# Optimization experiments

Measured on AMD Instinct MI355X. Metric: run time of the kernel, lower is better.

## Reference

```python
import jax, jax.numpy as jnp
import numpy as np

WS = 7    # window size
SS = 3    # shift size
NH = 6    # num heads
C = 192   # dim
HID = 768 # mlp hidden = 4*dim


def _rel_index():
    c = np.stack(np.meshgrid(np.arange(WS), np.arange(WS), indexing='ij')).reshape(2, -1)
    r = (c[:, :, None] - c[:, None, :]).transpose(1, 2, 0)
    r[..., 0] += WS - 1
    r[..., 1] += WS - 1
    r[..., 0] *= 2 * WS - 1
    return r.sum(-1)  # (49, 49) int


def _ln(x, g, b):
    m = jnp.mean(x, -1, keepdims=True)
    v = jnp.var(x, -1, keepdims=True)
    return (x - m) / jnp.sqrt(v + 1e-5) * g + b


def _wpart(x):
    B, H, W, c = x.shape
    return x.reshape(B, H // WS, WS, W // WS, WS, c).transpose(0, 1, 3, 2, 4, 5).reshape(-1, WS * WS, c)


def _wrev(w, H, W):
    B = w.shape[0] // ((H // WS) * (W // WS))
    return w.reshape(B, H // WS, W // WS, WS, WS, -1).transpose(0, 1, 3, 2, 4, 5).reshape(B, H, W, -1)


def setup_inputs() -> dict:
    key = jax.random.key(0)
    ks = jax.random.split(key, 40)
    it = iter(range(40))
    def nrm(shape, s=0.02):
        return jax.random.normal(ks[next(it)], shape, jnp.float32) * s
    B, H, W = 16, 56, 56
    L = H * W
    d = dict(se=nrm((B, L, C), 1.0), de=nrm((B, L, C), 1.0), co=nrm((B, L, C), 1.0))
    # shifted-window attention mask, exactly as Swin builds it
    img = np.zeros((1, H, W, 1), np.float32)
    cnt = 0
    for hs in (slice(0, -WS), slice(-WS, -SS), slice(-SS, None)):
        for cs in (slice(0, -WS), slice(-WS, -SS), slice(-SS, None)):
            img[:, hs, cs, :] = cnt
            cnt += 1
    mw = np.asarray(_wpart(jnp.asarray(img))).reshape(-1, WS * WS)  # (nW, 49)
    am = mw[:, None, :] - mw[:, :, None]
    d['mask_matrix'] = jnp.asarray(np.where(am != 0, -100.0, 0.0).astype(np.float32))
    d.update(
        n1se_g=jnp.ones(C), n1se_b=jnp.zeros(C), n1de_g=jnp.ones(C), n1de_b=jnp.zeros(C),
        rpb_table=nrm(((2 * WS - 1) ** 2, NH)),
        vse_w=nrm((2 * C, C)), vse_b=jnp.zeros(C), vde_w=nrm((2 * C, C)), vde_b=jnp.zeros(C),
        qk_w=nrm((C, 2 * C)), qk_b=jnp.zeros(2 * C),
        pse_w=nrm((C, C)), pse_b=jnp.zeros(C), pde_w=nrm((C, C)), pde_b=jnp.zeros(C),
        n2se_g=jnp.ones(C), n2se_b=jnp.zeros(C), n2de_g=jnp.ones(C), n2de_b=jnp.zeros(C),
        mse_w1=nrm((C, HID)), mse_b1=jnp.zeros(HID), mse_w2=nrm((HID, C)), mse_b2=jnp.zeros(C),
        mde_w1=nrm((C, HID)), mde_b1=jnp.zeros(HID), mde_w2=nrm((HID, C)), mde_b2=jnp.zeros(C),
        H=H, W=W)
    return d


def reference(se, de, co, mask_matrix,
              n1se_g, n1se_b, n1de_g, n1de_b, rpb_table,
              vse_w, vse_b, vde_w, vde_b, qk_w, qk_b,
              pse_w, pse_b, pde_w, pde_b,
              n2se_g, n2se_b, n2de_g, n2de_b,
              mse_w1, mse_b1, mse_w2, mse_b2,
              mde_w1, mde_b1, mde_w2, mde_b2,
              H, W):
    B, L, Cd = se.shape
    dh = Cd // NH
    scale = dh ** -0.5
    sc_se, sc_de = se, de
    se_n = _ln(se, n1se_g, n1se_b).reshape(B, H, W, Cd)
    de_n = _ln(de, n1de_g, n1de_b).reshape(B, H, W, Cd)
    co_n = co.reshape(B, H, W, Cd)  # co is not normed in the torch block
    # cyclic shift (H, W divisible by WS -> zero padding)
    se_s = jnp.roll(se_n, (-SS, -SS), (1, 2))
    de_s = jnp.roll(de_n, (-SS, -SS), (1, 2))
    co_s = jnp.roll(co_n, (-SS, -SS), (1, 2))
    sw, dw, cw = _wpart(se_s), _wpart(de_s), _wpart(co_s)  # (B_, N, C)
    B_, N, _ = sw.shape
    v_se = (jnp.concatenate([sw, cw], -1) @ vse_w + vse_b).reshape(B_, N, NH, dh).transpose(0, 2, 1, 3)
    v_de = (jnp.concatenate([dw, cw], -1) @ vde_w + vde_b).reshape(B_, N, NH, dh).transpose(0, 2, 1, 3)
    qk = (cw @ qk_w + qk_b).reshape(B_, N, 2, NH, dh).transpose(2, 0, 3, 1, 4)
    q, k = qk[0] * scale, qk[1]
    attn = jnp.einsum('bhnd,bhmd->bhnm', q, k)  # (B_, NH, N, N)
    bias = rpb_table[_rel_index().reshape(-1)].reshape(N, N, NH).transpose(2, 0, 1)
    attn = attn + bias[None]
    nW = mask_matrix.shape[0]
    attn = (attn.reshape(B_ // nW, nW, NH, N, N) + mask_matrix[None, :, None]).reshape(B_, NH, N, N)
    attn = jax.nn.softmax(attn, -1)
    se_o = jnp.einsum('bhnm,bhmd->bhnd', attn, v_se).transpose(0, 2, 1, 3).reshape(B_, N, Cd) @ pse_w + pse_b
    de_o = jnp.einsum('bhnm,bhmd->bhnd', attn, v_de).transpose(0, 2, 1, 3).reshape(B_, N, Cd) @ pde_w + pde_b
    se_r = jnp.roll(_wrev(se_o, H, W), (SS, SS), (1, 2)).reshape(B, L, Cd)
    de_r = jnp.roll(_wrev(de_o, H, W), (SS, SS), (1, 2)).reshape(B, L, Cd)
    se_out = sc_se + se_r
    de_out = sc_de + de_r
    se_out = se_out + (jax.nn.gelu(_ln(se_out, n2se_g, n2se_b) @ mse_w1 + mse_b1, approximate=False) @ mse_w2 + mse_b2)
    de_out = de_out + (jax.nn.gelu(_ln(de_out, n2de_g, n2de_b) @ mde_w1 + mde_b1, approximate=False) @ mde_w2 + mde_b2)
    return (se_out, de_out)
```

## Files before the change

kernel.cpp:

```cpp
#include <hip/hip_runtime.h>
#include <hip/hip_bf16.h>
#include <math.h>
#include <stdint.h>

typedef __hip_bfloat16 bf16;
typedef __attribute__((ext_vector_type(8))) short short8;
typedef __attribute__((ext_vector_type(4))) float f32x4;

#define B_SZ   16
#define HH     56
#define WW2    56
#define L_TOK  3136
#define C_DIM  192
#define NH_    6
#define DH     32
#define WS_    7
#define SS_    3
#define NW     49
#define NWIN   64
#define BWIN   (B_SZ*NWIN)
#define TOK    (BWIN*NW)
#define HID_   768

__device__ __forceinline__ float b2f(bf16 x){ return __bfloat162float(x); }
__device__ __forceinline__ bf16  f2b(float x){ return __float2bfloat16(x); }
__device__ __forceinline__ short f2bs(float x){ bf16 h = __float2bfloat16(x); return *reinterpret_cast<short*>(&h); }

__device__ __forceinline__ void gload16(const void* g, void* l) {
    __builtin_amdgcn_global_load_lds(
        (const __attribute__((address_space(1))) void*)(uintptr_t)g,
        (__attribute__((address_space(3))) void*)(uintptr_t)l, 16, 0, 0);
}

__device__ __forceinline__ float wave_sum64(float v){
    #pragma unroll
    for (int off = 32; off > 0; off >>= 1) v += __shfl_xor(v, off, 64);
    return v;
}

__global__ void prep_kernel(const float* __restrict__ se, const float* __restrict__ de,
                            const float* __restrict__ co,
                            const float* __restrict__ g1s, const float* __restrict__ b1s,
                            const float* __restrict__ g1d, const float* __restrict__ b1d,
                            bf16* __restrict__ sw, bf16* __restrict__ dw, bf16* __restrict__ cw)
{
    int t   = blockIdx.x;
    int tid = threadIdx.x;
    int b_  = t / NW, n = t % NW;
    int b   = b_ / NWIN, w = b_ % NWIN;
    int wh  = w >> 3, wwi = w & 7;
    int i   = n / WS_, j = n % WS_;
    int hs  = wh*WS_ + i, ws = wwi*WS_ + j;
    int hsrc = hs + SS_; if (hsrc >= HH)  hsrc -= HH;
    int wsrc = ws + SS_; if (wsrc >= WW2) wsrc -= WW2;
    long src = ((long)(b*L_TOK + hsrc*WW2 + wsrc)) * C_DIM;
    long dst = (long)t * C_DIM;

    {
        float x0 = se[src+tid], x1 = se[src+tid+64], x2 = se[src+tid+128];
        float s  = wave_sum64(x0+x1+x2);
        float ss = wave_sum64(x0*x0 + x1*x1 + x2*x2);
        float mean = s * (1.0f/192.0f);
        float var  = ss * (1.0f/192.0f) - mean*mean;
        float rstd = rsqrtf(var + 1e-5f);
        sw[dst+tid]     = f2b((x0-mean)*rstd*g1s[tid]     + b1s[tid]);
        sw[dst+tid+64]  = f2b((x1-mean)*rstd*g1s[tid+64]  + b1s[tid+64]);
        sw[dst+tid+128] = f2b((x2-mean)*rstd*g1s[tid+128] + b1s[tid+128]);
    }
    {
        float x0 = de[src+tid], x1 = de[src+tid+64], x2 = de[src+tid+128];
        float s  = wave_sum64(x0+x1+x2);
        float ss = wave_sum64(x0*x0 + x1*x1 + x2*x2);
        float mean = s * (1.0f/192.0f);
        float var  = ss * (1.0f/192.0f) - mean*mean;
        float rstd = rsqrtf(var + 1e-5f);
        dw[dst+tid]     = f2b((x0-mean)*rstd*g1d[tid]     + b1d[tid]);
        dw[dst+tid+64]  = f2b((x1-mean)*rstd*g1d[tid+64]  + b1d[tid+64]);
        dw[dst+tid+128] = f2b((x2-mean)*rstd*g1d[tid+128] + b1d[tid+128]);
    }
    cw[dst+tid]     = f2b(co[src+tid]);
    cw[dst+tid+64]  = f2b(co[src+tid+64]);
    cw[dst+tid+128] = f2b(co[src+tid+128]);
}

__global__ __launch_bounds__(256)
void wconv(const float* w0,const float* w1,const float* w2,const float* w3,const float* w4,
           const float* w5,const float* w6,const float* w7,const float* w8, short* dst)
{
    const float* src; int K, N; long doff;
    switch (blockIdx.y) {
      case 0: src=w0; K=384; N=192; doff=0;      break;
      case 1: src=w1; K=384; N=192; doff=73728;  break;
      case 2: src=w2; K=192; N=384; doff=147456; break;
      case 3: src=w3; K=192; N=192; doff=221184; break;
      case 4: src=w4; K=192; N=192; doff=258048; break;
      case 5: src=w5; K=192; N=768; doff=294912; break;
      case 6: src=w6; K=768; N=192; doff=442368; break;
      case 7: src=w7; K=192; N=768; doff=589824; break;
      default:src=w8; K=768; N=192; doff=737280; break;
    }
    int nblk = (K>>5)*(N>>6);
    int bid = blockIdx.x;
    if (bid >= nblk) return;
    int kb = bid / (N>>6), nb = bid % (N>>6);
    __shared__ float tile[32][65];
    int tid = threadIdx.x;
    #pragma unroll
    for (int it = 0; it < 8; ++it) {
        int idx = tid + it*256;
        int r = idx >> 6, c = idx & 63;
        tile[r][c] = src[(long)(kb*32 + r)*N + nb*64 + c];
    }
    __syncthreads();
    int lane = tid & 63, nl = tid >> 6;
    short8 v;
    #pragma unroll
    for (int j = 0; j < 8; ++j)
        v[j] = f2bs(tile[(lane>>4)*8 + j][nl*16 + (lane&15)]);
    long nig = (long)nb*4 + nl;
    *(short8*)(dst + doff + (((long)kb*(N>>4) + nig)*64 + lane)*8) = v;
}

template<int MODE, bool DUAL, int MR16>
__global__ __launch_bounds__(384)
void fgemm2(const bf16* __restrict__ A1, const bf16* __restrict__ A2, int K1, int K,
            const short* __restrict__ wf, const float* __restrict__ bias, int Nn,
            bf16* __restrict__ out, bf16* __restrict__ out2,
            const bf16* __restrict__ A1b, const bf16* __restrict__ A2b,
            const short* __restrict__ wfB, const float* __restrict__ biasB,
            bf16* __restrict__ outB, int nxblk)
{
    __shared__ short AsF[2][MR16][64][8];
    const int MROWS = MR16 * 16;
    const int MPW   = MR16 / 2;
    int tid = threadIdx.x;
    int wid = tid >> 6, lane = tid & 63;
    int wr = (wid >= 3) ? 1 : 0, wc = wid - wr*3;
    int l15 = lane & 15, g = lane >> 4;

    int bx = blockIdx.x;
    const bf16 *A1p = A1, *A2p = A2; const short* wfp = wf;
    const float* biasp = bias; bf16* outp = out;
    if (DUAL && bx >= nxblk) {
        bx -= nxblk; A1p = A1b; A2p = A2b; wfp = wfB; biasp = biasB; outp = outB;
    }
    int row0 = bx * MROWS, col0 = blockIdx.y * 192;
    const int ntiles = Nn >> 4;

    f32x4 acc[MPW][4];
    #pragma unroll
    for (int m = 0; m < MPW; m++)
        #pragma unroll
        for (int n = 0; n < 4; n++)
            acc[m][n] = (f32x4){0.f,0.f,0.f,0.f};

    int nk = K >> 5;
    #define STAGE(buf_, k0_) {                                                   \
        int colk = (k0_) + (g << 3);                                             \
        const bf16* asrc = (colk < K1) ? A1p : A2p;                              \
        int kc = (colk < K1) ? colk : colk - K1;                                 \
        if (wid < MR16)                                                          \
            gload16(asrc + (long)(row0 + wid*16 + l15)*K1 + kc,                  \
                    &AsF[buf_][wid][0][0]);                                      \
        if (MR16 == 8 && wid < 2)                                                \
            gload16(asrc + (long)(row0 + (6+wid)*16 + l15)*K1 + kc,              \
                    &AsF[buf_][(MR16==8 ? 6+wid : 0)][0][0]);                    \
    }

    STAGE(0, 0);
    __syncthreads();
    for (int t = 0; t < nk; ++t) {
        int buf = t & 1;
        if (t + 1 < nk) STAGE(buf ^ 1, (t+1) << 5);
        short8 af[MPW], bf4[4];
        #pragma unroll
        for (int m = 0; m < MPW; m++) af[m] = *((short8*)&AsF[buf][wr*MPW + m][lane][0]);
        const short* wbase = wfp + (((long)t*ntiles + (col0>>4) + wc*4)*64 + lane)*8;
        #pragma unroll
        for (int n = 0; n < 4; n++) bf4[n] = *(const short8*)(wbase + n*512);
        #pragma unroll
        for (int m = 0; m < MPW; m++)
            #pragma unroll
            for (int n = 0; n < 4; n++)
                acc[m][n] = __builtin_amdgcn_mfma_f32_16x16x32_bf16(af[m], bf4[n], acc[m][n], 0, 0, 0);
        __syncthreads();
    }
    #undef STAGE

    #pragma unroll
    for (int m = 0; m < MPW; m++) {
        #pragma unroll
        for (int rr = 0; rr < 4; rr++) {
            int t = row0 + wr*(MROWS/2) + m*16 + g*4 + rr;
            #pragma unroll
            for (int n2 = 0; n2 < 4; n2++) {
                int oc = col0 + wc*64 + n2*16 + l15;
                float v = acc[m][n2][rr] + biasp[oc];
                if (MODE == 0) {
                    outp[(long)t*Nn + oc] = f2b(v);
                } else if (MODE == 1) {
                    int b_ = t / NW, n = t % NW;
                    if (oc < C_DIM) {
                        int head = oc >> 5, d = oc & 31;
                        outp[(((long)b_*NH_ + head)*NW + n)*DH + d] = f2b(v * 0.17677669529663687f);
                    } else {
                        int och = oc - C_DIM;
                        int head = och >> 5, d = och & 31;
                        out2[(((long)b_*NH_ + head)*NW + n)*DH + d] = f2b(v);
                    }
                } else {
                    int b_ = t / NW, n = t % NW;
                    int head = oc >> 5, d = oc & 31;
                    outp[(((long)b_*NH_ + head)*NW + n)*DH + d] = f2b(v);
                }
            }
        }
    }
}

__global__ __launch_bounds__(384)
void pproj_ln2(const bf16* __restrict__ A, const short* __restrict__ wf,
               const float* __restrict__ bias, const float* __restrict__ res,
               const float* __restrict__ g2, const float* __restrict__ b2,
               bf16* __restrict__ x1o, bf16* __restrict__ xno,
               const bf16* __restrict__ Ab, const short* __restrict__ wfB,
               const float* __restrict__ biasB, const float* __restrict__ resB,
               const float* __restrict__ g2B, const float* __restrict__ b2B,
               bf16* __restrict__ x1oB, bf16* __restrict__ xnoB,
               int nxblk)
{
    __shared__ short AsFp[2][8][64][8];
    __shared__ float part[128][3][2];

    int tid = threadIdx.x;
    int wid = tid >> 6, lane = tid & 63;
    int wr = (wid >= 3) ? 1 : 0, wc = wid - wr*3;
    int l15 = lane & 15, g = lane >> 4;

    int bx = blockIdx.x;
    const bf16* Ap = A; const short* wfp = wf; const float* biasp = bias;
    const float* resp = res; const float* g2p = g2; const float* b2p = b2;
    bf16* x1p = x1o; bf16* xnp = xno;
    if (bx >= nxblk) {
        bx -= nxblk; Ap = Ab; wfp = wfB; biasp = biasB; resp = resB;
        g2p = g2B; b2p = b2B; x1p = x1oB; xnp = xnoB;
    }
    int row0 = bx * 128;

    f32x4 acc[4][4];
    #pragma unroll
    for (int m = 0; m < 4; m++)
        #pragma unroll
        for (int n = 0; n < 4; n++)
            acc[m][n] = (f32x4){0.f,0.f,0.f,0.f};

    #define PSTAGE(buf_, k0_) {                                                  \
        int colk = (k0_) + (g << 3);                                             \
        if (wid < 6)                                                             \
            gload16(Ap + (long)(row0 + wid*16 + l15)*C_DIM + colk,               \
                    &AsFp[buf_][wid][0][0]);                                     \
        if (wid < 2)                                                             \
            gload16(Ap + (long)(row0 + (6+wid)*16 + l15)*C_DIM + colk,           \
                    &AsFp[buf_][6+wid][0][0]);                                   \
    }

    PSTAGE(0, 0);
    __syncthreads();
    for (int t = 0; t < 6; ++t) {
        int buf = t & 1;
        if (t + 1 < 6) PSTAGE(buf ^ 1, (t+1) << 5);
        short8 af[4], bf4[4];
        #pragma unroll
        for (int m = 0; m < 4; m++)
            af[m] = *((short8*)&AsFp[buf][wr*4 + m][lane][0]);
        const short* wbase = wfp + (((long)t*12 + wc*4)*64 + lane)*8;
        #pragma unroll
        for (int n = 0; n < 4; n++) bf4[n] = *(const short8*)(wbase + n*512);
        #pragma unroll
        for (int m = 0; m < 4; m++)
            #pragma unroll
            for (int n = 0; n < 4; n++)
                acc[m][n] = __builtin_amdgcn_mfma_f32_16x16x32_bf16(af[m], bf4[n], acc[m][n], 0, 0, 0);
        __syncthreads();
    }
    #undef PSTAGE

    float bias4[4], g24[4], b24[4];
    #pragma unroll
    for (int n2 = 0; n2 < 4; n2++) {
        int oc = wc*64 + n2*16 + l15;
        bias4[n2] = biasp[oc]; g24[n2] = g2p[oc]; b24[n2] = b2p[oc];
    }

    int gtv[4][4];
    #pragma unroll
    for (int m = 0; m < 4; m++) {
        #pragma unroll
        for (int rr = 0; rr < 4; rr++) {
            int t = row0 + wr*64 + m*16 + g*4 + rr;
            int b_ = t / NW, n = t - b_*NW;
            int w = b_ & (NWIN-1), b = b_ >> 6;
            int hs = (w >> 3)*WS_ + n/WS_;
            int wsf = (w & 7)*WS_ + n % WS_;
            int h = hs + SS_;  if (h >= HH)  h -= HH;
            int wc2 = wsf + SS_; if (wc2 >= WW2) wc2 -= WW2;
            int gt = b*L_TOK + h*WW2 + wc2;
            gtv[m][rr] = gt;
            int lrow = wr*64 + m*16 + g*4 + rr;
            float ps = 0.f, pss = 0.f;
            #pragma unroll
            for (int n2 = 0; n2 < 4; n2++) {
                int oc = wc*64 + n2*16 + l15;
                float x1 = resp[(long)gt*C_DIM + oc] + acc[m][n2][rr] + bias4[n2];
                acc[m][n2][rr] = x1;
                x1p[(long)gt*C_DIM + oc] = f2b(x1);
                ps += x1; pss += x1*x1;
            }
            ps  += __shfl_xor(ps, 1);  pss += __shfl_xor(pss, 1);
            ps  += __shfl_xor(ps, 2);  pss += __shfl_xor(pss, 2);
            ps  += __shfl_xor(ps, 4);  pss += __shfl_xor(pss, 4);
            ps  += __shfl_xor(ps, 8);  pss += __shfl_xor(pss, 8);
            if (l15 == 0) {
                part[lrow][wc][0] = ps;
                part[lrow][wc][1] = pss;
            }
        }
    }
    __syncthreads();

    #pragma unroll
    for (int m = 0; m < 4; m++) {
        #pragma unroll
        for (int rr = 0; rr < 4; rr++) {
            int lrow = wr*64 + m*16 + g*4 + rr;
            int gt = gtv[m][rr];
            float s  = part[lrow][0][0] + part[lrow][1][0] + part[lrow][2][0];
            float ss = part[lrow][0][1] + part[lrow][1][1] + part[lrow][2][1];
            float mean = s * (1.0f/192.0f);
            float var  = ss * (1.0f/192.0f) - mean*mean;
            float rstd = rsqrtf(var + 1e-5f);
            #pragma unroll
            for (int n2 = 0; n2 < 4; n2++) {
                int oc = wc*64 + n2*16 + l15;
                xnp[(long)gt*C_DIM + oc] = f2b((acc[m][n2][rr] - mean)*rstd*g24[n2] + b24[n2]);
            }
        }
    }
}

__global__ __launch_bounds__(384)
void mlp_fused3(const bf16* __restrict__ xn, const short* __restrict__ w1f,
                const short* __restrict__ w2f,
                const float* __restrict__ b1, const float* __restrict__ b2,
                const bf16* __restrict__ x1, float* __restrict__ dout,
                const bf16* __restrict__ xnB, const short* __restrict__ w1B,
                const short* __restrict__ w2B,
                const float* __restrict__ b1B, const float* __restrict__ b2B,
                const bf16* __restrict__ x1B, float* __restrict__ doutB,
                int nxblk)
{
    __shared__ short xnF[24*512];
    __shared__ short hidS[2][24*512];

    int tid = threadIdx.x;
    int wv = tid >> 6, lane = tid & 63;
    int l15 = lane & 15, g = lane >> 4;

    int bx = blockIdx.x;
    const bf16* xnp = xn; const short* w1p = w1f; const short* w2p = w2f;
    const float* b1p = b1; const float* b2p = b2;
    const bf16* x1p = x1; float* doutp = dout;
    if (bx >= nxblk) {
        bx -= nxblk; xnp = xnB; w1p = w1B; w2p = w2B; b1p = b1B; b2p = b2B;
        x1p = x1B; doutp = doutB;
    }
    int row0 = bx * 64;

    #pragma unroll
    for (int p = 0; p < 4; ++p) {
        int pp = wv*4 + p;
        int a = pp / 6, kb = pp % 6;
        gload16(xnp + (long)(row0 + 16*a + l15)*C_DIM + 32*kb + 8*g,
                xnF + (a*6 + kb)*512);
    }
    __syncthreads();

    f32x4 ad[4][2], au[4][2];
    #pragma unroll
    for (int m = 0; m < 4; m++)
        #pragma unroll
        for (int n = 0; n < 2; n++)
            ad[m][n] = (f32x4){0.f,0.f,0.f,0.f};

    #define UP_SLICE(s_) {                                                       \
        _Pragma("unroll")                                                        \
        for (int m = 0; m < 4; m++)                                              \
            _Pragma("unroll")                                                    \
            for (int n = 0; n < 2; n++)                                          \
                au[m][n] = (f32x4){0.f,0.f,0.f,0.f};                             \
        _Pragma("unroll")                                                        \
        for (int kb = 0; kb < 6; ++kb) {                                         \
            short8 af[4];                                                        \
            _Pragma("unroll")                                                    \
            for (int m = 0; m < 4; m++)                                          \
                af[m] = *(short8*)(xnF + (m*6 + kb)*512 + lane*8);               \
            _Pragma("unroll")                                                    \
            for (int n = 0; n < 2; n++) {                                        \
                short8 bfv = *(const short8*)(w1p + (((long)kb*48 + 12*(s_) + 2*wv + n)*64 + lane)*8); \
                _Pragma("unroll")                                                \
                for (int m = 0; m < 4; m++)                                      \
                    au[m][n] = __builtin_amdgcn_mfma_f32_16x16x32_bf16(af[m], bfv, au[m][n], 0, 0, 0); \
            }                                                                    \
        }                                                                        \
    }

    #define SCATTER(s_, buf_) {                                                  \
        _Pragma("unroll")                                                        \
        for (int n = 0; n < 2; n++) {                                            \
            int hc = 32*wv + 16*n + l15;                                         \
            float bb = b1p[192*(s_) + hc];                                       \
            int kb2 = hc >> 5;                                                   \
            int Lhi = 16 * ((hc >> 3) & 3);                                      \
            int j = hc & 7;                                                      \
            _Pragma("unroll")                                                    \
            for (int m = 0; m < 4; m++) {                                        \
                _Pragma("unroll")                                                \
                for (int rr = 0; rr < 4; rr++) {                                 \
                    float v = au[m][n][rr] + bb;                                 \
                    float gl = 0.5f * v * (1.0f + erff(v * 0.70710678118654752f)); \
                    int L = (4*g + rr) + Lhi;                                    \
                    hidS[buf_][(m*6 + kb2)*512 + L*8 + j] = f2bs(gl);            \
                }                                                                \
            }                                                                    \
        }                                                                        \
    }

    #define DOWN_SLICE(s_, buf_) {                                               \
        _Pragma("unroll")                                                        \
        for (int kb = 0; kb < 6; ++kb) {                                         \
            short8 hf[4];                                                        \
            _Pragma("unroll")                                                    \
            for (int m = 0; m < 4; m++)                                          \
                hf[m] = *(short8*)(&hidS[buf_][(m*6 + kb)*512] + lane*8);        \
            _Pragma("unroll")                                                    \
            for (int n = 0; n < 2; n++) {                                        \
                short8 bfv = *(const short8*)(w2p + ((((long)(6*(s_) + kb))*12 + 2*wv + n)*64 + lane)*8); \
                _Pragma("unroll")                                                \
                for (int m = 0; m < 4; m++)                                      \
                    ad[m][n] = __builtin_amdgcn_mfma_f32_16x16x32_bf16(hf[m], bfv, ad[m][n], 0, 0, 0); \
            }                                                                    \
        }                                                                        \
    }

    UP_SLICE(0);
    SCATTER(0, 0);
    __syncthreads();
    UP_SLICE(1);
    DOWN_SLICE(0, 0);
    SCATTER(1, 1);
    __syncthreads();
    UP_SLICE(2);
    DOWN_SLICE(1, 1);
    SCATTER(2, 0);
    __syncthreads();
    UP_SLICE(3);
    DOWN_SLICE(2, 0);
    SCATTER(3, 1);
    __syncthreads();
    DOWN_SLICE(3, 1);

    #undef UP_SLICE
    #undef SCATTER
    #undef DOWN_SLICE

    #pragma unroll
    for (int m = 0; m < 4; m++) {
        #pragma unroll
        for (int rr = 0; rr < 4; rr++) {
            int t = row0 + 16*m + 4*g + rr;
            long goff = (long)t*C_DIM;
            #pragma unroll
            for (int n = 0; n < 2; n++) {
                int oc = 32*wv + 16*n + l15;
                float v = ad[m][n][rr] + b2p[oc];
                doutp[goff + oc] = b2f(x1p[goff + oc]) + v;
            }
        }
    }
}

#define BM 128
#define BN 64

template<int MODE>
__global__ __launch_bounds__(256)
void mgemm(const bf16* __restrict__ A1, const bf16* __restrict__ A2, int K1, int K,
           const float* __restrict__ W, const float* __restrict__ bias, int Nn,
           bf16* __restrict__ out, bf16* __restrict__ out2,
           const float* __restrict__ res_src, const bf16* __restrict__ prj,
           int t0, float* __restrict__ dout)
{
    __shared__ short AsF[8][64][8];
    __shared__ short BsF[4][64][8];
    int tid  = threadIdx.x;
    int wid  = tid >> 6, lane = tid & 63;
    int wr   = wid >> 1, wc = wid & 1;
    int row0 = blockIdx.x * BM, col0 = blockIdx.y * BN;

    f32x4 acc[4][2];
    #pragma unroll
    for (int m = 0; m < 4; m++)
        #pragma unroll
        for (int n = 0; n < 2; n++)
            acc[m][n] = (f32x4){0.f, 0.f, 0.f, 0.f};

    int ar = tid >> 2, akseg = tid & 3;
    int bc = tid & 63, bk8 = tid >> 6;

    for (int k0 = 0; k0 < K; k0 += 32) {
        {
            int col = k0 + akseg*8;
            const bf16* asrc = (col < K1) ? A1 : A2;
            int akc = (col < K1) ? col : col - K1;
            #pragma unroll
            for (int rr = 0; rr < 2; rr++) {
                int r = ar + rr*64;
                short8 av = *(const short8*)(asrc + (long)(row0 + r)*K1 + akc);
                *((short8*)&AsF[r >> 4][(r & 15) + (akseg << 4)][0]) = av;
            }
        }
        {
            short8 bv;
            #pragma unroll
            for (int j = 0; j < 8; j++)
                bv[j] = f2bs(W[(long)(k0 + bk8*8 + j)*Nn + col0 + bc]);
            *((short8*)&BsF[bc >> 4][(bc & 15) + (bk8 << 4)][0]) = bv;
        }
        __syncthreads();
        short8 af[4], bfr[2];
        #pragma unroll
        for (int m = 0; m < 4; m++) af[m]  = *((short8*)&AsF[wr*4 + m][lane][0]);
        #pragma unroll
        for (int n = 0; n < 2; n++) bfr[n] = *((short8*)&BsF[wc*2 + n][lane][0]);
        #pragma unroll
        for (int m = 0; m < 4; m++)
            #pragma unroll
            for (int n = 0; n < 2; n++)
                acc[m][n] = __builtin_amdgcn_mfma_f32_16x16x32_bf16(af[m], bfr[n], acc[m][n], 0, 0, 0);
        __syncthreads();
    }

    #pragma unroll
    for (int m = 0; m < 4; m++) {
        #pragma unroll
        for (int rr = 0; rr < 4; rr++) {
            int t = row0 + wr*64 + m*16 + (lane >> 4)*4 + rr;
            if (MODE == 4) {
                int tg = t0 + t;
                int b = tg / L_TOK, l = tg % L_TOK;
                int h = l / WW2, wcol = l % WW2;
                int hp = h - SS_;    if (hp < 0) hp += HH;
                int wp = wcol - SS_; if (wp < 0) wp += WW2;
                int b_ = b*NWIN + (hp/WS_)*8 + (wp/WS_);
                int n  = (hp%WS_)*WS_ + (wp%WS_);
                long wsoff = ((long)b_*NW + n)*C_DIM;
                long goff  = (long)tg*C_DIM;
                #pragma unroll
                for (int n2 = 0; n2 < 2; n2++) {
                    int oc = col0 + wc*32 + n2*16 + (lane & 15);
                    float v = acc[m][n2][rr] + bias[oc];
                    dout[goff + oc] = res_src[goff + oc] + b2f(prj[wsoff + oc]) + v;
                }
            } else {
                #pragma unroll
                for (int n2 = 0; n2 < 2; n2++) {
                    int oc = col0 + wc*32 + n2*16 + (lane & 15);
                    float v = acc[m][n2][rr] + bias[oc];
                    if (MODE == 0) {
                        out[(long)t*Nn + oc] = f2b(v);
                    } else if (MODE == 1) {
                        int b_ = t / NW, n = t % NW;
                        if (oc < C_DIM) {
                            int head = oc >> 5, d = oc & 31;
                            out[(((long)b_*NH_ + head)*NW + n)*DH + d] = f2b(v * 0.17677669529663687f);
                        } else {
                            int och = oc - C_DIM;
                            int head = och >> 5, d = och & 31;
                            out2[(((long)b_*NH_ + head)*NW + n)*DH + d] = f2b(v);
                        }
                    } else if (MODE == 2) {
                        int b_ = t / NW, n = t % NW;
                        int head = oc >> 5, d = oc & 31;
                        out[(((long)b_*NH_ + head)*NW + n)*DH + d] = f2b(v);
                    } else {
                        float g2 = 0.5f * v * (1.0f + erff(v * 0.70710678118654752f));
                        out[(long)t*Nn + oc] = f2b(g2);
                    }
                }
            }
        }
    }
}

#define PSTR 72
#define VSTR 72

__global__ __launch_bounds__(128)
void attn_mfma(const bf16* __restrict__ qb, const bf16* __restrict__ kb,
               const bf16* __restrict__ vse, const bf16* __restrict__ vde,
               const float* __restrict__ rpb,
               bf16* __restrict__ ose, bf16* __restrict__ ode)
{
    __shared__ float rpbs[169*NH_];
    __shared__ short P[2][64][PSTR];
    __shared__ short VTs[2][32][VSTR];
    __shared__ short VTd[2][32][VSTR];
    int tid = threadIdx.x, wid = tid >> 6, lane = tid & 63;
    for (int i = tid; i < 169*NH_; i += 128) rpbs[i] = rpb[i];
    __syncthreads();

    int bh = blockIdx.x*2 + wid;
    int b_ = bh / NH_, head = bh % NH_;
    int w = b_ & (NWIN-1);
    int wh = w >> 3, ww = w & 7;
    long base = (long)bh * (NW*DH);
    int l15 = lane & 15, g = lane >> 4;
    int j0 = lane >> 2, seg = lane & 3;

    short8 qf[4], kf[4], va_[4], vb_[4];
    #pragma unroll
    for (int mi = 0; mi < 4; mi++) {
        int r = l15 + 16*mi; if (r > 48) r = 48;
        qf[mi] = *(const short8*)(qb + base + r*DH + 8*g);
    }
    #pragma unroll
    for (int ni = 0; ni < 4; ni++) {
        int r = l15 + 16*ni; if (r > 48) r = 48;
        kf[ni] = *(const short8*)(kb + base + r*DH + 8*g);
    }
    #pragma unroll
    for (int it = 0; it < 4; ++it) {
        int j = j0 + 16*it;
        va_[it] = (short8){0,0,0,0,0,0,0,0};
        vb_[it] = (short8){0,0,0,0,0,0,0,0};
        if (j < NW) {
            va_[it] = *(const short8*)(vse + base + j*DH + seg*8);
            vb_[it] = *(const short8*)(vde + base + j*DH + seg*8);
        }
    }

    f32x4 sA[4][4];
    #pragma unroll
    for (int mi = 0; mi < 4; mi++)
        #pragma unroll
        for (int ni = 0; ni < 4; ni++)
            sA[mi][ni] = (f32x4){0.f,0.f,0.f,0.f};
    #pragma unroll
    for (int mi = 0; mi < 4; mi++)
        #pragma unroll
        for (int ni = 0; ni < 4; ni++)
            sA[mi][ni] = __builtin_amdgcn_mfma_f32_16x16x32_bf16(qf[mi], kf[ni], sA[mi][ni], 0, 0, 0);

    #pragma unroll
    for (int it = 0; it < 4; ++it) {
        int j = j0 + 16*it;
        #pragma unroll
        for (int s2 = 0; s2 < 8; ++s2) {
            VTs[wid][seg*8 + s2][j] = va_[it][s2];
            VTd[wid][seg*8 + s2][j] = vb_[it][s2];
        }
    }

    int jv[4], j7r_[4], j7c_[4], jrh_[4], jrc_[4];
    #pragma unroll
    for (int ni = 0; ni < 4; ++ni) {
        int j = 16*ni + l15;
        jv[ni] = (j < NW);
        int a = (j*37) >> 8; int c = j - 7*a;
        j7r_[ni] = a; j7c_[ni] = c;
        int jh = wh*7 + a, jw = ww*7 + c;
        jrh_[ni] = (jh >= 49) + (jh >= 53);
        jrc_[ni] = (jw >= 49) + (jw >= 53);
    }

    #pragma unroll
    for (int mi = 0; mi < 4; mi++) {
        #pragma unroll
        for (int rr = 0; rr < 4; rr++) {
            int i = 16*mi + 4*g + rr;
            int iv = (i < NW);
            int i7r = (i*37) >> 8; int i7c = i - 7*i7r;
            int ih = wh*7 + i7r, iw = ww*7 + i7c;
            int irh = (ih >= 49) + (ih >= 53), irc = (iw >= 49) + (iw >= 53);
            float e[4], sum = 0.f;
            #pragma unroll
            for (int ni = 0; ni < 4; ni++) {
                float sv;
                if (iv && jv[ni]) {
                    int ri = (i7r - j7r_[ni] + 6)*13 + (i7c - j7c_[ni] + 6);
                    float msk = (irh == jrh_[ni] && irc == jrc_[ni]) ? 0.f : -100.f;
                    sv = sA[mi][ni][rr] + rpbs[ri*NH_ + head] + msk;
                } else {
                    sv = -1e30f;
                }
                e[ni] = __expf(sv); sum += e[ni];
            }
            sum += __shfl_xor(sum, 1);
            sum += __shfl_xor(sum, 2);
            sum += __shfl_xor(sum, 4);
            sum += __shfl_xor(sum, 8);
            float inv = 1.0f / sum;
            #pragma unroll
            for (int ni = 0; ni < 4; ni++)
                P[wid][i][16*ni + l15] = f2bs(e[ni] * inv);
        }
    }
    __syncthreads();

    f32x4 o1[4][2], o2[4][2];
    #pragma unroll
    for (int mi = 0; mi < 4; mi++)
        #pragma unroll
        for (int di = 0; di < 2; di++) {
            o1[mi][di] = (f32x4){0.f,0.f,0.f,0.f};
            o2[mi][di] = (f32x4){0.f,0.f,0.f,0.f};
        }
    #pragma unroll
    for (int mi = 0; mi < 4; mi++) {
        #pragma unroll
        for (int kk = 0; kk < 2; kk++) {
            short8 ap = *((short8*)&P[wid][16*mi + l15][kk*32 + 8*g]);
            #pragma unroll
            for (int di = 0; di < 2; di++) {
                short8 bv1 = *((short8*)&VTs[wid][16*di + l15][kk*32 + 8*g]);
                o1[mi][di] = __builtin_amdgcn_mfma_f32_16x16x32_bf16(ap, bv1, o1[mi][di], 0, 0, 0);
                short8 bv2 = *((short8*)&VTd[wid][16*di + l15][kk*32 + 8*g]);
                o2[mi][di] = __builtin_amdgcn_mfma_f32_16x16x32_bf16(ap, bv2, o2[mi][di], 0, 0, 0);
            }
        }
    }

    #pragma unroll
    for (int mi = 0; mi < 4; mi++) {
        #pragma unroll
        for (int rr = 0; rr < 4; rr++) {
            int i = 16*mi + 4*g + rr;
            if (i < NW) {
                long ob = ((long)b_*NW + i)*C_DIM + head*DH;
                #pragma unroll
                for (int di = 0; di < 2; di++) {
                    ose[ob + 16*di + l15] = f2b(o1[mi][di][rr]);
                    ode[ob + 16*di + l15] = f2b(o2[mi][di][rr]);
                }
            }
        }
    }
}

__global__ void resid_ln2_kernel(const float* __restrict__ se, const float* __restrict__ de,
                                 const bf16* __restrict__ pse, const bf16* __restrict__ pde,
                                 const float* __restrict__ g2s, const float* __restrict__ bb2s,
                                 const float* __restrict__ g2d, const float* __restrict__ bb2d,
                                 bf16* __restrict__ xns, bf16* __restrict__ xnd)
{
    int t = blockIdx.x, tid = threadIdx.x;
    int b = t / L_TOK, l = t % L_TOK;
    int h = l / WW2, wc = l % WW2;
    int hp = h - SS_;  if (hp < 0) hp += HH;
    int wp = wc - SS_; if (wp < 0) wp += WW2;
    int b_ = b*NWIN + (hp/WS_)*8 + (wp/WS_);
    int n  = (hp%WS_)*WS_ + (wp%WS_);
    long wsoff = ((long)b_*NW + n)*C_DIM;
    long off   = (long)t*C_DIM;
    {
        float x0 = se[off+tid]     + b2f(pse[wsoff+tid]);
        float x1 = se[off+tid+64]  + b2f(pse[wsoff+tid+64]);
        float x2 = se[off+tid+128] + b2f(pse[wsoff+tid+128]);
        float s  = wave_sum64(x0+x1+x2);
        float ss = wave_sum64(x0*x0 + x1*x1 + x2*x2);
        float mean = s * (1.0f/192.0f);
        float var  = ss * (1.0f/192.0f) - mean*mean;
        float rstd = rsqrtf(var + 1e-5f);
        xns[off+tid]     = f2b((x0-mean)*rstd*g2s[tid]     + bb2s[tid]);
        xns[off+tid+64]  = f2b((x1-mean)*rstd*g2s[tid+64]  + bb2s[tid+64]);
        xns[off+tid+128] = f2b((x2-mean)*rstd*g2s[tid+128] + bb2s[tid+128]);
    }
    {
        float x0 = de[off+tid]     + b2f(pde[wsoff+tid]);
        float x1 = de[off+tid+64]  + b2f(pde[wsoff+tid+64]);
        float x2 = de[off+tid+128] + b2f(pde[wsoff+tid+128]);
        float s  = wave_sum64(x0+x1+x2);
        float ss = wave_sum64(x0*x0 + x1*x1 + x2*x2);
        float mean = s * (1.0f/192.0f);
        float var  = ss * (1.0f/192.0f) - mean*mean;
        float rstd = rsqrtf(var + 1e-5f);
        xnd[off+tid]     = f2b((x0-mean)*rstd*g2d[tid]     + bb2d[tid]);
        xnd[off+tid+64]  = f2b((x1-mean)*rstd*g2d[tid+64]  + bb2d[tid+64]);
        xnd[off+tid+128] = f2b((x2-mean)*rstd*g2d[tid+128] + bb2d[tid+128]);
    }
}

extern "C" void kernel_launch(void* const* d_in, const int* in_sizes, int n_in,
                              void* d_out, int out_size, void* d_ws, size_t ws_size,
                              hipStream_t stream)
{
    const float* se     = (const float*)d_in[0];
    const float* de     = (const float*)d_in[1];
    const float* co     = (const float*)d_in[2];
    const float* n1se_g = (const float*)d_in[4];
    const float* n1se_b = (const float*)d_in[5];
    const float* n1de_g = (const float*)d_in[6];
    const float* n1de_b = (const float*)d_in[7];
    const float* rpb    = (const float*)d_in[8];
    const float* vse_w  = (const float*)d_in[9];
    const float* vse_b  = (const float*)d_in[10];
    const float* vde_w  = (const float*)d_in[11];
    const float* vde_b  = (const float*)d_in[12];
    const float* qk_w   = (const float*)d_in[13];
    const float* qk_b   = (const float*)d_in[14];
    const float* pse_w  = (const float*)d_in[15];
    const float* pse_b  = (const float*)d_in[16];
    const float* pde_w  = (const float*)d_in[17];
    const float* pde_b  = (const float*)d_in[18];
    const float* n2se_g = (const float*)d_in[19];
    const float* n2se_b = (const float*)d_in[20];
    const float* n2de_g = (const float*)d_in[21];
    const float* n2de_b = (const float*)d_in[22];
    const float* mse_w1 = (const float*)d_in[23];
    const float* mse_b1 = (const float*)d_in[24];
    const float* mse_w2 = (const float*)d_in[25];
    const float* mse_b2 = (const float*)d_in[26];
    const float* mde_w1 = (const float*)d_in[27];
    const float* mde_b1 = (const float*)d_in[28];
    const float* mde_w2 = (const float*)d_in[29];
    const float* mde_b2 = (const float*)d_in[30];

    char* ws = (char*)d_ws;
    const size_t U = (size_t)TOK * C_DIM * 2;
    bf16* sw   = (bf16*)(ws + 0*U);
    bf16* dw   = (bf16*)(ws + 1*U);
    bf16* cw   = (bf16*)(ws + 2*U);
    bf16* vse  = (bf16*)(ws + 3*U);
    bf16* vde  = (bf16*)(ws + 4*U);
    bf16* ode  = (bf16*)(ws + 5*U);
    bf16* qb   = (bf16*)(ws + 0*U);
    bf16* kb   = (bf16*)(ws + 1*U);
    bf16* ose  = (bf16*)(ws + 2*U);
    bf16* x1se = (bf16*)(ws + 0*U);
    bf16* x1de = (bf16*)(ws + 1*U);
    bf16* xns  = (bf16*)(ws + 3*U);
    bf16* xnd  = (bf16*)(ws + 4*U);
    bf16* fb_pse = (bf16*)(ws + 0*U);
    bf16* fb_pde = (bf16*)(ws + 1*U);
    bf16* fb_xns = (bf16*)(ws + 2*U);
    bf16* fb_xnd = (bf16*)(ws + 3*U);
    bf16* fb_hid = (bf16*)(ws + 4*U);
    short* wfb = (short*)(ws + 6*U);

    const bool frag = (ws_size >= 6*U + 884736ull*2ull);
    float* dout = (float*)d_out;
    const int CH = TOK/2;
    const int NX = TOK/128;

    if (frag)
        wconv<<<dim3(72, 9), 256, 0, stream>>>(vse_w, vde_w, qk_w, pse_w, pde_w,
                                               mse_w1, mse_w2, mde_w1, mde_w2, wfb);
    prep_kernel<<<TOK, 64, 0, stream>>>(se, de, co, n1se_g, n1se_b, n1de_g, n1de_b, sw, dw, cw);

    if (frag) {
        fgemm2<2,true,8><<<dim3(NX*2, 1), 384, 0, stream>>>(sw, cw, C_DIM, 2*C_DIM, wfb + 0, vse_b, C_DIM,
                                                            vse, nullptr,
                                                            dw, cw, wfb + 73728, vde_b, vde, NX);
        fgemm2<1,false,8><<<dim3(NX, 2), 384, 0, stream>>>(cw, cw, C_DIM, C_DIM, wfb + 147456, qk_b, 384,
                                                           qb, kb,
                                                           nullptr, nullptr, nullptr, nullptr, nullptr, 0);
    } else {
        mgemm<2><<<dim3(TOK/BM, C_DIM/BN), 256, 0, stream>>>(sw, cw, C_DIM, 2*C_DIM, vse_w, vse_b, C_DIM,
                                                             vse, nullptr, nullptr, nullptr, 0, nullptr);
        mgemm<2><<<dim3(TOK/BM, C_DIM/BN), 256, 0, stream>>>(dw, cw, C_DIM, 2*C_DIM, vde_w, vde_b, C_DIM,
                                                             vde, nullptr, nullptr, nullptr, 0, nullptr);
        mgemm<1><<<dim3(TOK/BM, 384/BN), 256, 0, stream>>>(cw, cw, C_DIM, C_DIM, qk_w, qk_b, 384,
                                                           qb, kb, nullptr, nullptr, 0, nullptr);
    }

    attn_mfma<<<BWIN*NH_/2, 128, 0, stream>>>(qb, kb, vse, vde, rpb, ose, ode);

    if (frag) {
        pproj_ln2<<<dim3(NX*2, 1), 384, 0, stream>>>(ose, wfb + 221184, pse_b, se, n2se_g, n2se_b,
                                                     x1se, xns,
                                                     ode, wfb + 258048, pde_b, de, n2de_g, n2de_b,
                                                     x1de, xnd, NX);
        mlp_fused3<<<dim3((TOK/64)*2, 1), 384, 0, stream>>>(xns, wfb + 294912, wfb + 442368,
                                                            mse_b1, mse_b2, x1se, dout,
                                                            xnd, wfb + 589824, wfb + 737280,
                                                            mde_b1, mde_b2, x1de,
                                                            dout + (size_t)TOK*C_DIM, TOK/64);
    } else {
        mgemm<0><<<dim3(TOK/BM, C_DIM/BN), 256, 0, stream>>>(ose, ose, C_DIM, C_DIM, pse_w, pse_b, C_DIM,
                                                             fb_pse, nullptr, nullptr, nullptr, 0, nullptr);
        mgemm<0><<<dim3(TOK/BM, C_DIM/BN), 256, 0, stream>>>(ode, ode, C_DIM, C_DIM, pde_w, pde_b, C_DIM,
                                                             fb_pde, nullptr, nullptr, nullptr, 0, nullptr);
        resid_ln2_kernel<<<TOK, 64, 0, stream>>>(se, de, fb_pse, fb_pde,
                                                 n2se_g, n2se_b, n2de_g, n2de_b, fb_xns, fb_xnd);
        for (int c0 = 0; c0 < 2; c0++) {
            int t0 = c0 * CH;
            mgemm<3><<<dim3(CH/BM, HID_/BN), 256, 0, stream>>>(fb_xns + (long)t0*C_DIM, fb_xns + (long)t0*C_DIM,
                                                               C_DIM, C_DIM, mse_w1, mse_b1, HID_,
                                                               fb_hid, nullptr, nullptr, nullptr, 0, nullptr);
            mgemm<4><<<dim3(CH/BM, C_DIM/BN), 256, 0, stream>>>(fb_hid, fb_hid, HID_, HID_, mse_w2, mse_b2, C_DIM,
                                                                nullptr, nullptr, se, fb_pse, t0, dout);
        }
        for (int c0 = 0; c0 < 2; c0++) {
            int t0 = c0 * CH;
            mgemm<3><<<dim3(CH/BM, HID_/BN), 256, 0, stream>>>(fb_xnd + (long)t0*C_DIM, fb_xnd + (long)t0*C_DIM,
                                                               C_DIM, C_DIM, mde_w1, mde_b1, HID_,
                                                               fb_hid, nullptr, nullptr, nullptr, 0, nullptr);
            mgemm<4><<<dim3(CH/BM, C_DIM/BN), 256, 0, stream>>>(fb_hid, fb_hid, HID_, HID_, mde_w2, mde_b2, C_DIM,
                                                                nullptr, nullptr, de, fb_pde, t0,
                                                                dout + (size_t)TOK*C_DIM);
        }
    }
}
```

Baseline: 380.7 us.

## Halve MLP hidden slice width and add MFMA priority hints

```diff
diff --git a/kernel.cpp b/kernel.cpp
--- a/kernel.cpp
+++ b/kernel.cpp
@@ -178,11 +178,13 @@
         const short* wbase = wfp + (((long)t*ntiles + (col0>>4) + wc*4)*64 + lane)*8;
         #pragma unroll
         for (int n = 0; n < 4; n++) bf4[n] = *(const short8*)(wbase + n*512);
+        __builtin_amdgcn_s_setprio(1);
         #pragma unroll
         for (int m = 0; m < MPW; m++)
             #pragma unroll
             for (int n = 0; n < 4; n++)
                 acc[m][n] = __builtin_amdgcn_mfma_f32_16x16x32_bf16(af[m], bf4[n], acc[m][n], 0, 0, 0);
+        __builtin_amdgcn_s_setprio(0);
         __syncthreads();
     }
     #undef STAGE
@@ -276,11 +278,13 @@
         const short* wbase = wfp + (((long)t*12 + wc*4)*64 + lane)*8;
         #pragma unroll
         for (int n = 0; n < 4; n++) bf4[n] = *(const short8*)(wbase + n*512);
+        __builtin_amdgcn_s_setprio(1);
         #pragma unroll
         for (int m = 0; m < 4; m++)
             #pragma unroll
             for (int n = 0; n < 4; n++)
                 acc[m][n] = __builtin_amdgcn_mfma_f32_16x16x32_bf16(af[m], bf4[n], acc[m][n], 0, 0, 0);
+        __builtin_amdgcn_s_setprio(0);
         __syncthreads();
     }
     #undef PSTAGE
@@ -349,7 +353,7 @@
 }
 
 __global__ __launch_bounds__(384)
-void mlp_fused3(const bf16* __restrict__ xn, const short* __restrict__ w1f,
+void mlp_fused5(const bf16* __restrict__ xn, const short* __restrict__ w1f,
                 const short* __restrict__ w2f,
                 const float* __restrict__ b1, const float* __restrict__ b2,
                 const bf16* __restrict__ x1, float* __restrict__ dout,
@@ -360,7 +364,7 @@
                 int nxblk)
 {
     __shared__ short xnF[24*512];
-    __shared__ short hidS[2][24*512];
+    __shared__ short hidS[2][12*512];
 
     int tid = threadIdx.x;
     int wv = tid >> 6, lane = tid & 63;
@@ -385,7 +389,8 @@
     }
     __syncthreads();
 
-    f32x4 ad[4][2], au[4][2];
+    f32x4 ad[4][2];
+    f32x4 au[4];
     #pragma unroll
     for (int m = 0; m < 4; m++)
         #pragma unroll
@@ -394,80 +399,67 @@
 
     #define UP_SLICE(s_) {                                                       \
         _Pragma("unroll")                                                        \
-        for (int m = 0; m < 4; m++)                                              \
-            _Pragma("unroll")                                                    \
-            for (int n = 0; n < 2; n++)                                          \
-                au[m][n] = (f32x4){0.f,0.f,0.f,0.f};                             \
+        for (int m = 0; m < 4; m++) au[m] = (f32x4){0.f,0.f,0.f,0.f};            \
         _Pragma("unroll")                                                        \
         for (int kb = 0; kb < 6; ++kb) {                                         \
-            short8 af[4];                                                        \
+            short8 bfv = *(const short8*)(w1p + (((long)kb*48 + 6*(s_) + wv)*64 + lane)*8); \
+            __builtin_amdgcn_s_setprio(1);                                       \
             _Pragma("unroll")                                                    \
-            for (int m = 0; m < 4; m++)                                          \
-                af[m] = *(short8*)(xnF + (m*6 + kb)*512 + lane*8);               \
+            for (int m = 0; m < 4; m++) {                                        \
+                short8 af = *(short8*)(xnF + (m*6 + kb)*512 + lane*8);           \
+                au[m] = __builtin_amdgcn_mfma_f32_16x16x32_bf16(af, bfv, au[m], 0, 0, 0); \
+            }                                                                    \
+            __builtin_amdgcn_s_setprio(0);                                       \
+        }                                                                        \
+    }
+
+    #define SCATTER(s_, buf_) {                                                  \
+        int hc = 16*wv + l15;                                                    \
+        float bb = b1p[96*(s_) + hc];                                            \
+        int kb2 = hc >> 5;                                                       \
+        int Lhi = 16 * ((hc >> 3) & 3);                                          \
+        int j = hc & 7;                                                          \
+        _Pragma("unroll")                                                        \
+        for (int m = 0; m < 4; m++) {                                            \
             _Pragma("unroll")                                                    \
-            for (int n = 0; n < 2; n++) {                                        \
-                short8 bfv = *(const short8*)(w1p + (((long)kb*48 + 12*(s_) + 2*wv + n)*64 + lane)*8); \
-                _Pragma("unroll")                                                \
-                for (int m = 0; m < 4; m++)                                      \
-                    au[m][n] = __builtin_amdgcn_mfma_f32_16x16x32_bf16(af[m], bfv, au[m][n], 0, 0, 0); \
+            for (int rr = 0; rr < 4; rr++) {                                     \
+                float v = au[m][rr] + bb;                                        \
+                float gl = 0.5f * v * (1.0f + erff(v * 0.70710678118654752f));   \
+                int L = (4*g + rr) + Lhi;                                        \
+                hidS[buf_][(m*3 + kb2)*512 + L*8 + j] = f2bs(gl);                \
             }                                                                    \
         }                                                                        \
     }
 
-    #define SCATTER(s_, buf_) {                                                  \
-        _Pragma("unroll")                                                        \
-        for (int n = 0; n < 2; n++) {                                            \
-            int hc = 32*wv + 16*n + l15;                                         \
-            float bb = b1p[192*(s_) + hc];                                       \
-            int kb2 = hc >> 5;                                                   \
-            int Lhi = 16 * ((hc >> 3) & 3);                                      \
-            int j = hc & 7;                                                      \
-            _Pragma("unroll")                                                    \
-            for (int m = 0; m < 4; m++) {                                        \
-                _Pragma("unroll")                                                \
-                for (int rr = 0; rr < 4; rr++) {                                 \
-                    float v = au[m][n][rr] + bb;                                 \
-                    float gl = 0.5f * v * (1.0f + erff(v * 0.70710678118654752f)); \
-                    int L = (4*g + rr) + Lhi;                                    \
-                    hidS[buf_][(m*6 + kb2)*512 + L*8 + j] = f2bs(gl);            \
-                }                                                                \
-            }                                                                    \
-        }                                                                        \
-    }
-
     #define DOWN_SLICE(s_, buf_) {                                               \
         _Pragma("unroll")                                                        \
-        for (int kb = 0; kb < 6; ++kb) {                                         \
+        for (int kb = 0; kb < 3; ++kb) {                                         \
             short8 hf[4];                                                        \
             _Pragma("unroll")                                                    \
             for (int m = 0; m < 4; m++)                                          \
-                hf[m] = *(short8*)(&hidS[buf_][(m*6 + kb)*512] + lane*8);        \
+                hf[m] = *(short8*)(&hidS[buf_][(m*3 + kb)*512] + lane*8);        \
+            __builtin_amdgcn_s_setprio(1);                                       \
             _Pragma("unroll")                                                    \
             for (int n = 0; n < 2; n++) {                                        \
-                short8 bfv = *(const short8*)(w2p + ((((long)(6*(s_) + kb))*12 + 2*wv + n)*64 + lane)*8); \
+                short8 bfv = *(const short8*)(w2p + ((((long)(3*(s_) + kb))*12 + 2*wv + n)*64 + lane)*8); \
                 _Pragma("unroll")                                                \
                 for (int m = 0; m < 4; m++)                                      \
                     ad[m][n] = __builtin_amdgcn_mfma_f32_16x16x32_bf16(hf[m], bfv, ad[m][n], 0, 0, 0); \
             }                                                                    \
+            __builtin_amdgcn_s_setprio(0);                                       \
         }                                                                        \
     }
 
     UP_SLICE(0);
     SCATTER(0, 0);
     __syncthreads();
-    UP_SLICE(1);
-    DOWN_SLICE(0, 0);
-    SCATTER(1, 1);
-    __syncthreads();
-    UP_SLICE(2);
-    DOWN_SLICE(1, 1);
-    SCATTER(2, 0);
-    __syncthreads();
-    UP_SLICE(3);
-    DOWN_SLICE(2, 0);
-    SCATTER(3, 1);
-    __syncthreads();
-    DOWN_SLICE(3, 1);
+    for (int s = 1; s < 8; ++s) {
+        UP_SLICE(s);
+        DOWN_SLICE(s-1, (s-1)&1);
+        SCATTER(s, s&1);
+        __syncthreads();
+    }
+    DOWN_SLICE(7, 1);
 
     #undef UP_SLICE
     #undef SCATTER
@@ -890,7 +882,7 @@
                                                      x1se, xns,
                                                      ode, wfb + 258048, pde_b, de, n2de_g, n2de_b,
                                                      x1de, xnd, NX);
-        mlp_fused3<<<dim3((TOK/64)*2, 1), 384, 0, stream>>>(xns, wfb + 294912, wfb + 442368,
+        mlp_fused5<<<dim3((TOK/64)*2, 1), 384, 0, stream>>>(xns, wfb + 294912, wfb + 442368,
                                                             mse_b1, mse_b2, x1se, dout,
                                                             xnd, wfb + 589824, wfb + 737280,
                                                             mde_b1, mde_b2, x1de,
```

Result: faster. 368.1 us (-3.3%).
